# Performance work log

Measured on AMD Instinct MI355X. Metric: run time of the kernel, lower is better.

The kernel has to match this reference:

```python
import jax, jax.numpy as jnp
import numpy as np

B, S, D, H, R = 16, 2048, 1024, 1024, 16


def setup_inputs() -> dict:
    key = jax.random.key(0)
    ks = jax.random.split(key, 6)
    inv = 1.0 / np.sqrt(D)
    return {
        "x": jax.random.normal(ks[0], (B, S, D), jnp.float32),
        "Wa": jax.random.uniform(ks[1], (H, D), jnp.float32, -inv, inv),
        "ba": jnp.zeros((H,), jnp.float32),
        "Wg": jax.random.uniform(ks[2], (R, D), jnp.float32, -inv, inv),
        "bg": jnp.zeros((R,), jnp.float32),
        "Wu": jax.random.uniform(ks[3], (H, D), jnp.float32, -inv, inv),
        "bu": jnp.zeros((H,), jnp.float32),
        "u": jax.random.normal(ks[4], (H, R), jnp.float32) * 0.02,
        "v": jax.random.normal(ks[5], (H, R), jnp.float32) * 0.02,
    }


def reference(x, Wa, ba, Wg, bg, Wu, bu, u, v):
    # Precompute all per-step projections in big GEMMs (same math as the
    # per-step Linear calls in the original loop).
    a = jax.nn.sigmoid(jnp.einsum('bsd,hd->bsh', x, Wa) + ba)   # [B,S,H]
    g = jnp.einsum('bsd,rd->bsr', x, Wg) + bg                    # [B,S,R]
    u_in = jnp.einsum('bsd,hd->bsh', x, Wu) + bu                 # [B,S,H]

    def step(state, ins):
        a_t, g_t, u_t = ins                      # [B,H], [B,R], [B,H]
        low_rank = (state @ v) * g_t             # [B,R]
        state = a_t * state + u_t + low_rank @ u.T
        return state, None

    init = jnp.zeros((x.shape[0], Wa.shape[0]), x.dtype)
    seq = (jnp.swapaxes(a, 0, 1), jnp.swapaxes(g, 0, 1), jnp.swapaxes(u_in, 0, 1))
    state, _ = jax.lax.scan(step, init, seq)
    return state  # [B, H]
```

## Files before the change

### kernel.cpp

```cpp
#include <hip/hip_runtime.h>
#include <hip/hip_bf16.h>
#include <stdint.h>

#define Bb 16
#define Ss 2048
#define Dd 1024
#define Hh 1024
#define Rr 16
#define Mm 32768

typedef __attribute__((ext_vector_type(4))) float f32x4;
typedef __attribute__((ext_vector_type(8))) short bf16x8;
typedef __attribute__((ext_vector_type(2))) _Float16 h2;

__device__ __forceinline__ unsigned short f2bf(float f) {
    union { float f; uint32_t u; } c; c.f = f;
    uint32_t u = c.u + 0x7fffu + ((c.u >> 16) & 1u);
    return (unsigned short)(u >> 16);
}
__device__ __forceinline__ float bfbits2f(uint32_t bits) {
    union { uint32_t u; float f; } c; c.u = bits << 16; return c.f;
}
__device__ __forceinline__ h2 u2h(unsigned int x) {
    union { unsigned int u; h2 h; } c; c.u = x; return c.h;
}
__device__ __forceinline__ h2 mkh2(float a, float b) {
    h2 r; r.x = (_Float16)a; r.y = (_Float16)b; return r;
}

__device__ __forceinline__ float DOT2(h2 a, h2 b, float c) {
#if __has_builtin(__builtin_amdgcn_fdot2)
    return __builtin_amdgcn_fdot2(a, b, c, false);
#else
    return fmaf((float)a.x, (float)b.x, fmaf((float)a.y, (float)b.y, c));
#endif
}

__device__ __forceinline__ void gld16(const void* gsrc, void* ldst) {
    __builtin_amdgcn_global_load_lds(
        (const __attribute__((address_space(1))) unsigned int*)gsrc,
        (__attribute__((address_space(3))) unsigned int*)ldst, 16, 0, 0);
}

__device__ __forceinline__ void softbar() {
    __asm volatile("" ::: "memory");
    __builtin_amdgcn_s_waitcnt(0xC07F);
    __builtin_amdgcn_s_barrier();
    __asm volatile("" ::: "memory");
}

__global__ __launch_bounds__(256) void k_convert(
    const float* __restrict__ x, const float* __restrict__ Wa,
    const float* __restrict__ Wu,
    unsigned short* __restrict__ xb, unsigned short* __restrict__ Wab,
    unsigned short* __restrict__ Wub)
{
    long e = ((long)blockIdx.x * 256 + threadIdx.x) * 4;
    const long nx = (long)Mm * Dd;
    const long nw = (long)Hh * Dd;
    const float* src; unsigned short* dst; long o;
    if (e < nx)            { src = x;  dst = xb;  o = e; }
    else if (e < nx + nw)  { src = Wa; dst = Wab; o = e - nx; }
    else                   { src = Wu; dst = Wub; o = e - nx - nw; }
    float4 f = *(const float4*)(src + o);
    ushort4 r;
    r.x = f2bf(f.x); r.y = f2bf(f.y); r.z = f2bf(f.z); r.w = f2bf(f.w);
    *(ushort4*)(dst + o) = r;
}

__global__ __launch_bounds__(256) void k_gemm(
    const unsigned short* __restrict__ Xb,
    const unsigned short* __restrict__ Wab,
    const unsigned short* __restrict__ Wub,
    const float* __restrict__ ba, const float* __restrict__ bu,
    unsigned short* __restrict__ outA, unsigned short* __restrict__ outU)
{
    __shared__ short At[128 * 32];
    __shared__ short Bt[128 * 32];

    const int tid  = threadIdx.x;
    const int lane = tid & 63;
    const int wave = tid >> 6;
    const int bm = blockIdx.x;
    const int bn = blockIdx.y;
    const int region = bn >> 3;
    const int nbase = (bn & 7) * 128;

    const short* Ag = (const short*)Xb;
    const short* Bg = (const short*)(region ? Wub : Wab);
    const float* bias = region ? bu : ba;
    unsigned short* outp = region ? outU : outA;

    const int wm = wave & 1, wn = wave >> 1;
    const int srow = lane >> 2, sseg = lane & 3;
    const int mrow = lane & 15, kb = lane >> 4;

    f32x4 acc[4][4] = {};

    for (int kt = 0; kt < 32; ++kt) {
        __syncthreads();
        const int k0 = kt * 32;
        #pragma unroll
        for (int p = 0; p < 2; ++p) {
            const int row = p * 64 + wave * 16 + srow;
            const short* ga = Ag + (long)(bm * 128 + row) * Dd + k0 + sseg * 8;
            gld16((const void*)ga, (void*)&At[p * 2048 + wave * 512]);
            const short* gb = Bg + (long)(nbase + row) * Dd + k0 + sseg * 8;
            gld16((const void*)gb, (void*)&Bt[p * 2048 + wave * 512]);
        }
        __syncthreads();

        bf16x8 af[4], bq[4];
        #pragma unroll
        for (int i = 0; i < 4; ++i) {
            af[i] = *(const bf16x8*)&At[(wm * 64 + i * 16 + mrow) * 32 + kb * 8];
            bq[i] = *(const bf16x8*)&Bt[(wn * 64 + i * 16 + mrow) * 32 + kb * 8];
        }
        #pragma unroll
        for (int i = 0; i < 4; ++i)
            #pragma unroll
            for (int j = 0; j < 4; ++j)
                acc[i][j] = __builtin_amdgcn_mfma_f32_16x16x32_bf16(
                    af[i], bq[j], acc[i][j], 0, 0, 0);
    }

    const int col = lane & 15, rq = lane >> 4;
    #pragma unroll
    for (int j = 0; j < 4; ++j) {
        const int n = nbase + wn * 64 + j * 16 + col;
        const float bv = bias[n];
        #pragma unroll
        for (int i = 0; i < 4; ++i) {
            const int mb = bm * 128 + wm * 64 + i * 16 + rq * 4;
            #pragma unroll
            for (int r = 0; r < 4; ++r) {
                float vv = acc[i][j][r] + bv;
                if (region == 0) vv = 1.0f / (1.0f + __expf(-vv));
                outp[(long)(mb + r) * Hh + n] = f2bf(vv);
            }
        }
    }
}

__global__ __launch_bounds__(256) void k_g(
    const float* __restrict__ x, const float* __restrict__ Wg,
    const float* __restrict__ bg, float* __restrict__ g)
{
    const int tid = threadIdx.x;
    const int r = tid & 15, ml = tid >> 4;
    const long m = (long)blockIdx.x * 16 + ml;
    const float4* xr = (const float4*)(x + m * Dd);
    const float4* wr = (const float4*)(Wg + (long)r * Dd);
    float acc = 0.0f;
    #pragma unroll 4
    for (int k = 0; k < Dd / 4; ++k) {
        float4 a = xr[k], b = wr[k];
        acc = fmaf(a.x, b.x, acc); acc = fmaf(a.y, b.y, acc);
        acc = fmaf(a.z, b.z, acc); acc = fmaf(a.w, b.w, acc);
    }
    g[m * Rr + r] = acc + bg[r];
}

__global__ __launch_bounds__(1024) void k_scan(
    const unsigned short* __restrict__ a,
    const unsigned short* __restrict__ uin,
    const float* __restrict__ g,
    const float* __restrict__ u,
    const float* __restrict__ v,
    float* __restrict__ out)
{
    __shared__ __align__(16) _Float16 sh[Hh];
    __shared__ __align__(16) float cacc[16 * 20];
    __shared__ __align__(16) _Float16 qh[16];

    const int tid  = threadIdx.x;
    const int lane = tid & 63;
    const int wave = tid >> 6;
    const int sub  = lane >> 4;
    const int ra   = lane & 15;
    const int b = blockIdx.x;

    const int hA = wave * 64 + sub * 16;
    h2 vr2[8];
    #pragma unroll
    for (int j = 0; j < 8; ++j)
        vr2[j] = mkh2(v[(hA + 2 * j) * Rr + ra], v[(hA + 2 * j + 1) * Rr + ra]);
    h2 ur2[8];
    #pragma unroll
    for (int j = 0; j < 4; ++j) {
        float4 t4 = *(const float4*)&u[tid * Rr + j * 4];
        ur2[2 * j]     = mkh2(t4.x, t4.y);
        ur2[2 * j + 1] = mkh2(t4.z, t4.w);
    }

    const unsigned short* ap = a   + (long)b * Ss * Hh + tid;
    const unsigned short* up = uin + (long)b * Ss * Hh + tid;
    const float*          gp = g   + (long)b * Ss * Rr + tid;

    float s = 0.0f;
    uint32_t pa[4], pu[4]; float pg[4];
    #pragma unroll
    for (int t = 0; t < 4; ++t) { pa[t] = ap[t * Hh]; pu[t] = up[t * Hh]; }
    ap += 4 * Hh; up += 4 * Hh;
    if (tid < 16) {
        #pragma unroll
        for (int t = 0; t < 4; ++t) pg[t] = gp[t * Rr];
        gp += 4 * Rr;
    }

    sh[tid] = (_Float16)0.0f;
    __syncthreads();

    const _Float16* spA16 = &sh[hA];

#define STEP(R, PF) do {                                                    \
                   \
    uint4 sA = *(const uint4*)(spA16);                                      \
    uint4 sB = *(const uint4*)(spA16 + 8);                                  \
    float part;                                                             \
    part = DOT2(u2h(sA.x), vr2[0], 0.0f);                                   \
    part = DOT2(u2h(sA.y), vr2[1], part);                                   \
    part = DOT2(u2h(sA.z), vr2[2], part);                                   \
    part = DOT2(u2h(sA.w), vr2[3], part);                                   \
    part = DOT2(u2h(sB.x), vr2[4], part);                                   \
    part = DOT2(u2h(sB.y), vr2[5], part);                                   \
    part = DOT2(u2h(sB.z), vr2[6], part);                                   \
    part = DOT2(u2h(sB.w), vr2[7], part);                                   \
    part += __shfl_xor(part, 16);                                           \
    part += __shfl_xor(part, 32);                                           \
    if (lane < 16) cacc[20 * ra + wave] = part;                             \
    softbar();                                                    \
               \
    if (tid < 16) {                                                         \
        const float* cr = &cacc[20 * tid];                                  \
        f32x4 c0 = *(const f32x4*)(cr);                                     \
        f32x4 c1 = *((const f32x4*)(cr) + 1);                               \
        f32x4 c2 = *((const f32x4*)(cr) + 2);                               \
        f32x4 c3 = *((const f32x4*)(cr) + 3);                               \
        f32x4 cs = (c0 + c1) + (c2 + c3);                                   \
        qh[tid] = (_Float16)(pg[R] * ((cs.x + cs.y) + (cs.z + cs.w)));      \
        if (PF) { pg[R] = *gp; gp += Rr; }                                  \
    }                                                                       \
    softbar();                                                    \
        \
    uint4 qA = *(const uint4*)(qh);                                         \
    uint4 qB = *(const uint4*)(qh + 8);                                     \
    float lr;                                                               \
    lr = DOT2(u2h(qA.x), ur2[0], 0.0f);                                     \
    lr = DOT2(u2h(qA.y), ur2[1], lr);                                       \
    lr = DOT2(u2h(qA.z), ur2[2], lr);                                       \
    lr = DOT2(u2h(qA.w), ur2[3], lr);                                       \
    lr = DOT2(u2h(qB.x), ur2[4], lr);                                       \
    lr = DOT2(u2h(qB.y), ur2[5], lr);                                       \
    lr = DOT2(u2h(qB.z), ur2[6], lr);                                       \
    lr = DOT2(u2h(qB.w), ur2[7], lr);                                       \
    s = fmaf(bfbits2f(pa[R]), s, bfbits2f(pu[R]) + lr);                     \
    sh[tid] = (_Float16)s;                                                  \
    if (PF) {                                                               \
        pa[R] = *ap; ap += Hh;                                              \
        pu[R] = *up; up += Hh;                                              \
    }                                                                       \
    softbar();                                                    \
} while (0)

    for (int t4 = 0; t4 < Ss / 4 - 1; ++t4) {
        STEP(0, 1); STEP(1, 1); STEP(2, 1); STEP(3, 1);
    }
    STEP(0, 0); STEP(1, 0); STEP(2, 0); STEP(3, 0);
#undef STEP

    out[(long)b * Hh + tid] = s;
}

extern "C" void kernel_launch(void* const* d_in, const int* in_sizes, int n_in,
                              void* d_out, int out_size, void* d_ws, size_t ws_size,
                              hipStream_t stream)
{
    const float* x  = (const float*)d_in[0];
    const float* Wa = (const float*)d_in[1];
    const float* ba = (const float*)d_in[2];
    const float* Wg = (const float*)d_in[3];
    const float* bg = (const float*)d_in[4];
    const float* Wu = (const float*)d_in[5];
    const float* bu = (const float*)d_in[6];
    const float* u  = (const float*)d_in[7];
    const float* v  = (const float*)d_in[8];
    float* out = (float*)d_out;

    char* ws = (char*)d_ws;
    unsigned short* xb   = (unsigned short*)(ws);
    unsigned short* Wab  = (unsigned short*)(ws + 67108864);
    unsigned short* Wub  = (unsigned short*)(ws + 69206016);
    unsigned short* abuf = (unsigned short*)(ws + 71303168);
    unsigned short* ubuf = (unsigned short*)(ws + 138412032);
    float*          gbuf = (float*)(ws + 205520896);

    hipLaunchKernelGGL(k_convert, dim3(34816), dim3(256), 0, stream,
                       x, Wa, Wu, xb, Wab, Wub);
    hipLaunchKernelGGL(k_gemm, dim3(256, 16), dim3(256), 0, stream,
                       xb, Wab, Wub, ba, bu, abuf, ubuf);
    hipLaunchKernelGGL(k_g, dim3(2048), dim3(256), 0, stream,
                       x, Wg, bg, gbuf);
    hipLaunchKernelGGL(k_scan, dim3(Bb), dim3(1024), 0, stream,
                       abuf, ubuf, gbuf, u, v, out);
}
```

Before: 1.826 ms.

## Halve scan block to 512 threads with two hidden units per thread and DPP reductions

The sequential scan kernel now uses 512 threads per batch, and each thread owns two adjacent state elements. Each wave handles 128 hidden rows and computes both halves of the rank-16 projection, with a DPP cross-lane exchange replacing part of the shuffle reduction. Partial sums are stored in LDS as fp16, and the u-projection is split across thread pairs and combined with DPP. This targets barrier and latency cost per step in the serial loop. The price is more register work per thread and extra fp16 rounding of the partial sums.

```diff
diff --git a/kernel.cpp b/kernel.cpp
--- a/kernel.cpp
+++ b/kernel.cpp
@@ -34,6 +34,15 @@
 #else
     return fmaf((float)a.x, (float)b.x, fmaf((float)a.y, (float)b.y, c));
 #endif
+}
+
+__device__ __forceinline__ float dpp_xor8(float x) {
+    return __int_as_float(__builtin_amdgcn_mov_dpp(
+        __float_as_int(x), 0x128, 0xF, 0xF, false));
+}
+__device__ __forceinline__ float dpp_xor1(float x) {
+    return __int_as_float(__builtin_amdgcn_mov_dpp(
+        __float_as_int(x), 0xB1, 0xF, 0xF, false));
 }
 
 __device__ __forceinline__ void gld16(const void* gsrc, void* ldst) {
@@ -161,7 +170,7 @@
     g[m * Rr + r] = acc + bg[r];
 }
 
-__global__ __launch_bounds__(1024) void k_scan(
+__global__ __launch_bounds__(512) void k_scan(
     const unsigned short* __restrict__ a,
     const unsigned short* __restrict__ uin,
     const float* __restrict__ g,
@@ -170,97 +179,131 @@
     float* __restrict__ out)
 {
     __shared__ __align__(16) _Float16 sh[Hh];
-    __shared__ __align__(16) float cacc[16 * 20];
-    __shared__ __align__(16) _Float16 qh[16];
+    __shared__ __align__(16) _Float16 cacc[16 * 8];
+    __shared__ __align__(32) _Float16 qh[16];
 
     const int tid  = threadIdx.x;
     const int lane = tid & 63;
     const int wave = tid >> 6;
-    const int sub  = lane >> 4;
-    const int ra   = lane & 15;
+    const int oA   = lane >> 3;
+    const int pA   = lane & 7;
+    const int side = tid & 1;
     const int b = blockIdx.x;
 
-    const int hA = wave * 64 + sub * 16;
-    h2 vr2[8];
+    const int h0 = 2 * tid;
+    const int hW = wave * 128 + oA * 16;
+    h2 vrA[8], vrB[8];
     #pragma unroll
-    for (int j = 0; j < 8; ++j)
-        vr2[j] = mkh2(v[(hA + 2 * j) * Rr + ra], v[(hA + 2 * j + 1) * Rr + ra]);
-    h2 ur2[8];
+    for (int k = 0; k < 8; ++k) {
+        vrA[k] = mkh2(v[(hW + 2 * k) * Rr + pA],
+                      v[(hW + 2 * k + 1) * Rr + pA]);
+        vrB[k] = mkh2(v[(hW + 2 * k) * Rr + pA + 8],
+                      v[(hW + 2 * k + 1) * Rr + pA + 8]);
+    }
+    const int hp0 = 2 * (tid ^ 1);
+    h2 ur00[4], ur01[4], urP0[4], urP1[4];
     #pragma unroll
-    for (int j = 0; j < 4; ++j) {
-        float4 t4 = *(const float4*)&u[tid * Rr + j * 4];
-        ur2[2 * j]     = mkh2(t4.x, t4.y);
-        ur2[2 * j + 1] = mkh2(t4.z, t4.w);
-    }
-
-    const unsigned short* ap = a   + (long)b * Ss * Hh + tid;
-    const unsigned short* up = uin + (long)b * Ss * Hh + tid;
-    const float*          gp = g   + (long)b * Ss * Rr + tid;
-
-    float s = 0.0f;
+    for (int k = 0; k < 4; ++k) {
+        const int r0 = 8 * side + 2 * k;
+        ur00[k] = mkh2(u[(h0)     * Rr + r0], u[(h0)     * Rr + r0 + 1]);
+        ur01[k] = mkh2(u[(h0 + 1) * Rr + r0], u[(h0 + 1) * Rr + r0 + 1]);
+        urP0[k] = mkh2(u[(hp0)     * Rr + r0], u[(hp0)     * Rr + r0 + 1]);
+        urP1[k] = mkh2(u[(hp0 + 1) * Rr + r0], u[(hp0 + 1) * Rr + r0 + 1]);
+    }
+
+    const uint32_t* apu = (const uint32_t*)(a   + (long)b * Ss * Hh) + tid;
+    const uint32_t* upu = (const uint32_t*)(uin + (long)b * Ss * Hh) + tid;
+    const float*    gp  = g + (long)b * Ss * Rr + tid;
+
+    float s0 = 0.0f, s1 = 0.0f;
     uint32_t pa[4], pu[4]; float pg[4];
     #pragma unroll
-    for (int t = 0; t < 4; ++t) { pa[t] = ap[t * Hh]; pu[t] = up[t * Hh]; }
-    ap += 4 * Hh; up += 4 * Hh;
+    for (int t = 0; t < 4; ++t) { pa[t] = apu[t * 512]; pu[t] = upu[t * 512]; }
+    apu += 4 * 512; upu += 4 * 512;
     if (tid < 16) {
         #pragma unroll
         for (int t = 0; t < 4; ++t) pg[t] = gp[t * Rr];
         gp += 4 * Rr;
     }
 
-    sh[tid] = (_Float16)0.0f;
+    ((uint32_t*)sh)[tid] = 0u;
     __syncthreads();
 
-    const _Float16* spA16 = &sh[hA];
+    const _Float16* spA = &sh[hW];
+    const _Float16* qpC = &qh[8 * side];
+    const h2 one2 = mkh2(1.0f, 1.0f);
 
 #define STEP(R, PF) do {                                                    \
-                   \
-    uint4 sA = *(const uint4*)(spA16);                                      \
-    uint4 sB = *(const uint4*)(spA16 + 8);                                  \
-    float part;                                                             \
-    part = DOT2(u2h(sA.x), vr2[0], 0.0f);                                   \
-    part = DOT2(u2h(sA.y), vr2[1], part);                                   \
-    part = DOT2(u2h(sA.z), vr2[2], part);                                   \
-    part = DOT2(u2h(sA.w), vr2[3], part);                                   \
-    part = DOT2(u2h(sB.x), vr2[4], part);                                   \
-    part = DOT2(u2h(sB.y), vr2[5], part);                                   \
-    part = DOT2(u2h(sB.z), vr2[6], part);                                   \
-    part = DOT2(u2h(sB.w), vr2[7], part);                                   \
-    part += __shfl_xor(part, 16);                                           \
-    part += __shfl_xor(part, 32);                                           \
-    if (lane < 16) cacc[20 * ra + wave] = part;                             \
-    softbar();                                                    \
+           \
+    uint4 sA = *(const uint4*)(spA);                                        \
+    uint4 sB = *(const uint4*)(spA + 8);                                    \
+    float lo, hi;                                                           \
+    lo = DOT2(u2h(sA.x), vrA[0], 0.0f);                                     \
+    lo = DOT2(u2h(sA.y), vrA[1], lo);                                       \
+    lo = DOT2(u2h(sA.z), vrA[2], lo);                                       \
+    lo = DOT2(u2h(sA.w), vrA[3], lo);                                       \
+    lo = DOT2(u2h(sB.x), vrA[4], lo);                                       \
+    lo = DOT2(u2h(sB.y), vrA[5], lo);                                       \
+    lo = DOT2(u2h(sB.z), vrA[6], lo);                                       \
+    lo = DOT2(u2h(sB.w), vrA[7], lo);                                       \
+    hi = DOT2(u2h(sA.x), vrB[0], 0.0f);                                     \
+    hi = DOT2(u2h(sA.y), vrB[1], hi);                                       \
+    hi = DOT2(u2h(sA.z), vrB[2], hi);                                       \
+    hi = DOT2(u2h(sA.w), vrB[3], hi);                                       \
+    hi = DOT2(u2h(sB.x), vrB[4], hi);                                       \
+    hi = DOT2(u2h(sB.y), vrB[5], hi);                                       \
+    hi = DOT2(u2h(sB.z), vrB[6], hi);                                       \
+    hi = DOT2(u2h(sB.w), vrB[7], hi);                                       \
+     \
+    {                                                                       \
+        float tlo = dpp_xor8(lo), thi = dpp_xor8(hi);                       \
+        float v1 = (lane & 8) ? (hi + thi) : (lo + tlo);                    \
+        v1 += __shfl_xor(v1, 16);                                           \
+        v1 += __shfl_xor(v1, 32);                                           \
+        if (lane < 16) cacc[lane * 8 + wave] = (_Float16)v1;                \
+    }                                                                       \
+               \
+    float a0 = bfbits2f(pa[R] & 0xFFFFu), a1 = bfbits2f(pa[R] >> 16);       \
+    float u0 = bfbits2f(pu[R] & 0xFFFFu), u1 = bfbits2f(pu[R] >> 16);       \
+    if (PF) {                                                               \
+        pa[R] = *apu; apu += 512;                                           \
+        pu[R] = *upu; upu += 512;                                           \
+    }                                                                       \
+    softbar();                                      \
                \
     if (tid < 16) {                                                         \
-        const float* cr = &cacc[20 * tid];                                  \
-        f32x4 c0 = *(const f32x4*)(cr);                                     \
-        f32x4 c1 = *((const f32x4*)(cr) + 1);                               \
-        f32x4 c2 = *((const f32x4*)(cr) + 2);                               \
-        f32x4 c3 = *((const f32x4*)(cr) + 3);                               \
-        f32x4 cs = (c0 + c1) + (c2 + c3);                                   \
-        qh[tid] = (_Float16)(pg[R] * ((cs.x + cs.y) + (cs.z + cs.w)));      \
+        uint4 c = *(const uint4*)&cacc[tid * 8];                            \
+        float ssum;                                                         \
+        ssum = DOT2(u2h(c.x), one2, 0.0f);                                  \
+        ssum = DOT2(u2h(c.y), one2, ssum);                                  \
+        ssum = DOT2(u2h(c.z), one2, ssum);                                  \
+        ssum = DOT2(u2h(c.w), one2, ssum);                                  \
+        qh[tid] = (_Float16)(pg[R] * ssum);                                 \
         if (PF) { pg[R] = *gp; gp += Rr; }                                  \
     }                                                                       \
-    softbar();                                                    \
-        \
-    uint4 qA = *(const uint4*)(qh);                                         \
-    uint4 qB = *(const uint4*)(qh + 8);                                     \
-    float lr;                                                               \
-    lr = DOT2(u2h(qA.x), ur2[0], 0.0f);                                     \
-    lr = DOT2(u2h(qA.y), ur2[1], lr);                                       \
-    lr = DOT2(u2h(qA.z), ur2[2], lr);                                       \
-    lr = DOT2(u2h(qA.w), ur2[3], lr);                                       \
-    lr = DOT2(u2h(qB.x), ur2[4], lr);                                       \
-    lr = DOT2(u2h(qB.y), ur2[5], lr);                                       \
-    lr = DOT2(u2h(qB.z), ur2[6], lr);                                       \
-    lr = DOT2(u2h(qB.w), ur2[7], lr);                                       \
-    s = fmaf(bfbits2f(pa[R]), s, bfbits2f(pu[R]) + lr);                     \
-    sh[tid] = (_Float16)s;                                                  \
-    if (PF) {                                                               \
-        pa[R] = *ap; ap += Hh;                                              \
-        pu[R] = *up; up += Hh;                                              \
+    softbar();                                        \
+     \
+                 \
+    uint4 q4 = *(const uint4*)qpC;                                          \
+    h2 q0 = u2h(q4.x), q1 = u2h(q4.y), q2 = u2h(q4.z), q3 = u2h(q4.w);     \
+    float pO0 = DOT2(q0, ur00[0],                                           \
+                DOT2(q1, ur00[1], DOT2(q2, ur00[2], DOT2(q3, ur00[3], 0.0f))));\
+    float pO1 = DOT2(q0, ur01[0],                                           \
+                DOT2(q1, ur01[1], DOT2(q2, ur01[2], DOT2(q3, ur01[3], 0.0f))));\
+    float pP0 = DOT2(q0, urP0[0],                                           \
+                DOT2(q1, urP0[1], DOT2(q2, urP0[2], DOT2(q3, urP0[3], 0.0f))));\
+    float pP1 = DOT2(q0, urP1[0],                                           \
+                DOT2(q1, urP1[1], DOT2(q2, urP1[2], DOT2(q3, urP1[3], 0.0f))));\
+    float lr0 = pO0 + dpp_xor1(pP0);                                        \
+    float lr1 = pO1 + dpp_xor1(pP1);                                        \
+    s0 = fmaf(a0, s0, u0 + lr0);                                            \
+    s1 = fmaf(a1, s1, u1 + lr1);                                            \
+    {                                                                       \
+        union { _Float16 h[2]; uint32_t u32; } pk;                          \
+        pk.h[0] = (_Float16)s0; pk.h[1] = (_Float16)s1;                     \
+        ((uint32_t*)sh)[tid] = pk.u32;                                      \
     }                                                                       \
-    softbar();                                                    \
+    softbar();                                     \
 } while (0)
 
     for (int t4 = 0; t4 < Ss / 4 - 1; ++t4) {
@@ -269,7 +312,7 @@
     STEP(0, 0); STEP(1, 0); STEP(2, 0); STEP(3, 0);
 #undef STEP
 
-    out[(long)b * Hh + tid] = s;
+    *(float2*)(out + (long)b * Hh + h0) = make_float2(s0, s1);
 }
 
 extern "C" void kernel_launch(void* const* d_in, const int* in_sizes, int n_in,
@@ -301,6 +344,6 @@
                        xb, Wab, Wub, ba, bu, abuf, ubuf);
     hipLaunchKernelGGL(k_g, dim3(2048), dim3(256), 0, stream,
                        x, Wg, bg, gbuf);
-    hipLaunchKernelGGL(k_scan, dim3(Bb), dim3(1024), 0, stream,
+    hipLaunchKernelGGL(k_scan, dim3(Bb), dim3(512), 0, stream,
                        abuf, ubuf, gbuf, u, v, out);
 }
```

Measured after the change: 1.858 ms. About the same (+1.7%).
